# Kernel optimization log

Hardware: AMD Instinct MI355X
Metric: run time of the kernel (lower is better)

The kernel has to match this reference:

```python
import jax, jax.numpy as jnp
import numpy as np

B, C, L = 16, 256, 1024
DIM_U, Q_EMB = 64, 64
INTER = DIM_U * Q_EMB  # 4096
EPS = 1e-5

def setup_inputs() -> dict:
    key = jax.random.key(0)
    ks = jax.random.split(key, 7)
    x = jax.random.normal(ks[0], (B, C, L), dtype=jnp.float32)
    u_i = jax.random.normal(ks[1], (B, DIM_U), dtype=jnp.float32)
    e_qid = jax.random.normal(ks[2], (B, Q_EMB, L), dtype=jnp.float32)
    t = jax.random.normal(ks[3], (B, 1, L), dtype=jnp.float32)
    # nn.Linear weights: (out_features, in_features), Kaiming-uniform-ish init
    wb = 1.0 / np.sqrt(INTER)
    W = jax.random.uniform(ks[4], (2 * C, INTER), jnp.float32, -wb, wb)
    V = jax.random.uniform(ks[5], (2 * C, 1), jnp.float32, -1.0, 1.0)
    bias = jnp.zeros((2 * C,), dtype=jnp.float32)
    return {"x": x, "u_i": u_i, "e_qid": e_qid, "t": t, "W": W, "V": V, "bias": bias}

def reference(x, u_i, e_qid, t, W, V, bias):
    # InstanceNorm1d (affine=False): per-(b,c) stats over L, biased variance
    mean = jnp.mean(x, axis=-1, keepdims=True)
    var = jnp.mean(jnp.square(x - mean), axis=-1, keepdims=True)
    nx = (x - mean) * jax.lax.rsqrt(var + EPS)
    # Bilinear conditioning: interaction[b, u*Q+q, l] = u_i[b,u] * e_qid[b,q,l];
    # style = W @ interaction, fused as a single contraction (no BxINTERxL tensor)
    Wr = W.reshape(2 * C, DIM_U, Q_EMB)
    style = jnp.einsum('bu,bql,cuq->bcl', u_i, e_qid, Wr)  # (B, 2C, L)
    time = jnp.einsum('bol,co->bcl', t, V)                  # (B, 2C, L)
    params = style + time + bias[None, :, None]
    gamma, beta = jnp.split(params, 2, axis=1)
    return (1.0 + gamma) * nx + beta
```

## Files before the change

kernel.cpp:

```cpp
#include <hip/hip_runtime.h>

#define NB 16
#define NC 256
#define NL 1024
#define NQ 64
#define NU 64
#define N2C 512
#define NINTER 4096
#define CT 32
#define LT 128

__global__ __launch_bounds__(256) void calc_A_kernel(
    const float* __restrict__ u_i, const float* __restrict__ W,
    float* __restrict__ A) {
  __shared__ float su[NB * NU];
  __shared__ float part[4][NB][NQ];
  const int t = threadIdx.x;
  const int c2 = blockIdx.x;
  const int q = t & 63;
  const int u4 = t >> 6;

#pragma unroll
  for (int k = 0; k < 4; ++k) su[t + k * 256] = u_i[t + k * 256];
  __syncthreads();

  float acc[NB];
#pragma unroll
  for (int b = 0; b < NB; ++b) acc[b] = 0.0f;

  const float* Wrow = W + c2 * NINTER + u4 * 16 * NQ;
#pragma unroll
  for (int uu = 0; uu < 16; ++uu) {
    const float w = Wrow[uu * NQ + q];
    const int u = u4 * 16 + uu;
#pragma unroll
    for (int b = 0; b < NB; ++b) acc[b] = fmaf(su[b * NU + u], w, acc[b]);
  }
#pragma unroll
  for (int b = 0; b < NB; ++b) part[u4][b][q] = acc[b];
  __syncthreads();

#pragma unroll
  for (int i = 0; i < 4; ++i) {
    const int b = (t >> 6) * 4 + i;
    const float s = part[0][b][q] + part[1][b][q] + part[2][b][q] + part[3][b][q];
    A[(b * N2C + c2) * NQ + q] = s;
  }
}

__global__ __launch_bounds__(256) void stats_kernel(
    const float* __restrict__ x, float* __restrict__ mean,
    float* __restrict__ rstd) {
  const int row = blockIdx.x;
  const int t = threadIdx.x;
  const float4 v = reinterpret_cast<const float4*>(x)[row * (NL / 4) + t];
  float s = v.x + v.y + v.z + v.w;
  float ss = v.x * v.x + v.y * v.y + v.z * v.z + v.w * v.w;
#pragma unroll
  for (int off = 32; off >= 1; off >>= 1) {
    s += __shfl_xor(s, off, 64);
    ss += __shfl_xor(ss, off, 64);
  }
  __shared__ float ls[4], lss[4];
  const int w = t >> 6;
  if ((t & 63) == 0) { ls[w] = s; lss[w] = ss; }
  __syncthreads();
  if (t == 0) {
    const float S = ls[0] + ls[1] + ls[2] + ls[3];
    const float SS = lss[0] + lss[1] + lss[2] + lss[3];
    const float m = S * (1.0f / NL);
    const float var = SS * (1.0f / NL) - m * m;
    mean[row] = m;
    rstd[row] = rsqrtf(var + 1e-5f);
  }
}

__device__ __forceinline__ void fma4(float4& acc, float a, const float4& e) {
  acc.x = fmaf(a, e.x, acc.x);
  acc.y = fmaf(a, e.y, acc.y);
  acc.z = fmaf(a, e.z, acc.z);
  acc.w = fmaf(a, e.w, acc.w);
}

__global__ __launch_bounds__(256) void fused_kernel(
    const float* __restrict__ x, const float* __restrict__ e,
    const float* __restrict__ tt, const float* __restrict__ V,
    const float* __restrict__ bias, const float* __restrict__ A,
    const float* __restrict__ mean, const float* __restrict__ rstd,
    float* __restrict__ out) {
  __shared__ float Ag[CT][NQ];
  __shared__ float Ab[CT][NQ];
  __shared__ float sm[CT], sr[CT];

  const int blk = blockIdx.x;
  const int b = blk >> 6;
  const int ct = (blk >> 3) & 7;
  const int lt = blk & 7;
  const int t = threadIdx.x;
  const int col = t & 31;
  const int rg = t >> 5;

  {
    const float4* Asg =
        reinterpret_cast<const float4*>(A + (b * N2C + ct * CT) * NQ);
    const float4* Asb =
        reinterpret_cast<const float4*>(A + (b * N2C + NC + ct * CT) * NQ);
    float4* Agv = reinterpret_cast<float4*>(&Ag[0][0]);
    float4* Abv = reinterpret_cast<float4*>(&Ab[0][0]);
#pragma unroll
    for (int k = 0; k < 2; ++k) {
      Agv[t + k * 256] = Asg[t + k * 256];
      Abv[t + k * 256] = Asb[t + k * 256];
    }
  }
  if (t < CT) {
    sm[t] = mean[b * NC + ct * CT + t];
    sr[t] = rstd[b * NC + ct * CT + t];
  }
  __syncthreads();

  float4 g[4], p[4];
#pragma unroll
  for (int i = 0; i < 4; ++i) {
    g[i] = make_float4(0.f, 0.f, 0.f, 0.f);
    p[i] = make_float4(0.f, 0.f, 0.f, 0.f);
  }

  const float* ebase = e + b * NQ * NL + lt * LT;
#pragma unroll 4
  for (int q0 = 0; q0 < NQ; q0 += 4) {
    const float4 e0 = reinterpret_cast<const float4*>(ebase + (q0 + 0) * NL)[col];
    const float4 e1 = reinterpret_cast<const float4*>(ebase + (q0 + 1) * NL)[col];
    const float4 e2 = reinterpret_cast<const float4*>(ebase + (q0 + 2) * NL)[col];
    const float4 e3 = reinterpret_cast<const float4*>(ebase + (q0 + 3) * NL)[col];
#pragma unroll
    for (int i = 0; i < 4; ++i) {
      const int r = rg * 4 + i;
      const float4 a = *reinterpret_cast<const float4*>(&Ag[r][q0]);
      fma4(g[i], a.x, e0);
      fma4(g[i], a.y, e1);
      fma4(g[i], a.z, e2);
      fma4(g[i], a.w, e3);
      const float4 c = *reinterpret_cast<const float4*>(&Ab[r][q0]);
      fma4(p[i], c.x, e0);
      fma4(p[i], c.y, e1);
      fma4(p[i], c.z, e2);
      fma4(p[i], c.w, e3);
    }
  }

  const float4 tv = reinterpret_cast<const float4*>(tt + b * NL + lt * LT)[col];
#pragma unroll
  for (int i = 0; i < 4; ++i) {
    const int r = rg * 4 + i;
    const int c = ct * CT + r;
    const float vg = V[c], vb = V[c + NC];
    const float bg = bias[c], bb = bias[c + NC];
    const float m = sm[r], rs = sr[r];
    const float4 xv =
        reinterpret_cast<const float4*>(x + (b * NC + c) * NL + lt * LT)[col];
    float4 o;
    const float gx = 1.0f + g[i].x + fmaf(tv.x, vg, bg);
    const float gy = 1.0f + g[i].y + fmaf(tv.y, vg, bg);
    const float gz = 1.0f + g[i].z + fmaf(tv.z, vg, bg);
    const float gw = 1.0f + g[i].w + fmaf(tv.w, vg, bg);
    o.x = fmaf(gx, (xv.x - m) * rs, p[i].x + fmaf(tv.x, vb, bb));
    o.y = fmaf(gy, (xv.y - m) * rs, p[i].y + fmaf(tv.y, vb, bb));
    o.z = fmaf(gz, (xv.z - m) * rs, p[i].z + fmaf(tv.z, vb, bb));
    o.w = fmaf(gw, (xv.w - m) * rs, p[i].w + fmaf(tv.w, vb, bb));
    reinterpret_cast<float4*>(out + (b * NC + c) * NL + lt * LT)[col] = o;
  }
}

extern "C" void kernel_launch(void* const* d_in, const int* in_sizes, int n_in,
                              void* d_out, int out_size, void* d_ws,
                              size_t ws_size, hipStream_t stream) {
  const float* x = (const float*)d_in[0];
  const float* u_i = (const float*)d_in[1];
  const float* e = (const float*)d_in[2];
  const float* tt = (const float*)d_in[3];
  const float* W = (const float*)d_in[4];
  const float* V = (const float*)d_in[5];
  const float* bias = (const float*)d_in[6];
  float* out = (float*)d_out;

  float* A = (float*)d_ws;
  float* mean = A + NB * N2C * NQ;
  float* rstd = mean + NB * NC;

  calc_A_kernel<<<N2C, 256, 0, stream>>>(u_i, W, A);
  stats_kernel<<<NB * NC, 256, 0, stream>>>(x, mean, rstd);
  fused_kernel<<<NB * 64, 256, 0, stream>>>(x, e, tt, V, bias, A, mean, rstd,
                                            out);
}
```

Before: 108.5 us.

## Fuse instance-norm stats into main kernel and tile full L rows per block

Removes the separate stats kernel. Each fused block now loads 8 full channel rows of x into shared memory, computes mean and rstd there, and reuses the staged x in the epilogue. Blocks now cover the whole L dimension with 8 channels instead of 32 channels by 128 positions. This cuts one launch and the second global read of x. In exchange it uses 32KB of LDS per block, holds 16 float4 accumulators per thread, and launches half as many blocks (512).

```diff
diff --git a/kernel.cpp b/kernel.cpp
--- a/kernel.cpp
+++ b/kernel.cpp
@@ -7,8 +7,7 @@
 #define NU 64
 #define N2C 512
 #define NINTER 4096
-#define CT 32
-#define LT 128
+#define CB 8
 
 __global__ __launch_bounds__(256) void calc_A_kernel(
     const float* __restrict__ u_i, const float* __restrict__ W,
@@ -43,35 +42,9 @@
 #pragma unroll
   for (int i = 0; i < 4; ++i) {
     const int b = (t >> 6) * 4 + i;
-    const float s = part[0][b][q] + part[1][b][q] + part[2][b][q] + part[3][b][q];
+    const float s =
+        part[0][b][q] + part[1][b][q] + part[2][b][q] + part[3][b][q];
     A[(b * N2C + c2) * NQ + q] = s;
-  }
-}
-
-__global__ __launch_bounds__(256) void stats_kernel(
-    const float* __restrict__ x, float* __restrict__ mean,
-    float* __restrict__ rstd) {
-  const int row = blockIdx.x;
-  const int t = threadIdx.x;
-  const float4 v = reinterpret_cast<const float4*>(x)[row * (NL / 4) + t];
-  float s = v.x + v.y + v.z + v.w;
-  float ss = v.x * v.x + v.y * v.y + v.z * v.z + v.w * v.w;
-#pragma unroll
-  for (int off = 32; off >= 1; off >>= 1) {
-    s += __shfl_xor(s, off, 64);
-    ss += __shfl_xor(ss, off, 64);
-  }
-  __shared__ float ls[4], lss[4];
-  const int w = t >> 6;
-  if ((t & 63) == 0) { ls[w] = s; lss[w] = ss; }
-  __syncthreads();
-  if (t == 0) {
-    const float S = ls[0] + ls[1] + ls[2] + ls[3];
-    const float SS = lss[0] + lss[1] + lss[2] + lss[3];
-    const float m = S * (1.0f / NL);
-    const float var = SS * (1.0f / NL) - m * m;
-    mean[row] = m;
-    rstd[row] = rsqrtf(var + 1e-5f);
   }
 }
 
@@ -86,89 +59,90 @@
     const float* __restrict__ x, const float* __restrict__ e,
     const float* __restrict__ tt, const float* __restrict__ V,
     const float* __restrict__ bias, const float* __restrict__ A,
-    const float* __restrict__ mean, const float* __restrict__ rstd,
     float* __restrict__ out) {
-  __shared__ float Ag[CT][NQ];
-  __shared__ float Ab[CT][NQ];
-  __shared__ float sm[CT], sr[CT];
+  __shared__ float xs[CB][NL];
+  __shared__ float As[2 * CB][NQ];
+  __shared__ float sm[CB], sr[CB];
 
   const int blk = blockIdx.x;
-  const int b = blk >> 6;
-  const int ct = (blk >> 3) & 7;
-  const int lt = blk & 7;
+  const int b = blk >> 5;
+  const int c0 = (blk & 31) * CB;
   const int t = threadIdx.x;
-  const int col = t & 31;
-  const int rg = t >> 5;
 
   {
-    const float4* Asg =
-        reinterpret_cast<const float4*>(A + (b * N2C + ct * CT) * NQ);
-    const float4* Asb =
-        reinterpret_cast<const float4*>(A + (b * N2C + NC + ct * CT) * NQ);
-    float4* Agv = reinterpret_cast<float4*>(&Ag[0][0]);
-    float4* Abv = reinterpret_cast<float4*>(&Ab[0][0]);
+    const int fr = t >> 4;
+    const int fc = t & 15;
+    const int ar = (fr < CB) ? (c0 + fr) : (NC + c0 + fr - CB);
+    *reinterpret_cast<float4*>(&As[fr][fc * 4]) =
+        reinterpret_cast<const float4*>(A + (b * N2C + ar) * NQ)[fc];
+  }
+
+  {
+    const int rw = t >> 5;
+    const int cl = t & 31;
+    const float* xrow = x + (b * NC + c0 + rw) * NL;
+    float s = 0.0f, ss = 0.0f;
 #pragma unroll
-    for (int k = 0; k < 2; ++k) {
-      Agv[t + k * 256] = Asg[t + k * 256];
-      Abv[t + k * 256] = Asb[t + k * 256];
+    for (int k = 0; k < 8; ++k) {
+      const float4 v = reinterpret_cast<const float4*>(xrow)[cl + 32 * k];
+      *reinterpret_cast<float4*>(&xs[rw][(cl + 32 * k) * 4]) = v;
+      s += (v.x + v.y) + (v.z + v.w);
+      ss = fmaf(v.x, v.x, fmaf(v.y, v.y, fmaf(v.z, v.z, fmaf(v.w, v.w, ss))));
     }
-  }
-  if (t < CT) {
-    sm[t] = mean[b * NC + ct * CT + t];
-    sr[t] = rstd[b * NC + ct * CT + t];
+#pragma unroll
+    for (int off = 16; off >= 1; off >>= 1) {
+      s += __shfl_xor(s, off, 64);
+      ss += __shfl_xor(ss, off, 64);
+    }
+    if (cl == 0) {
+      const float m = s * (1.0f / NL);
+      sm[rw] = m;
+      sr[rw] = rsqrtf(ss * (1.0f / NL) - m * m + 1e-5f);
+    }
   }
   __syncthreads();
 
-  float4 g[4], p[4];
+  float4 acc[2 * CB];
 #pragma unroll
-  for (int i = 0; i < 4; ++i) {
-    g[i] = make_float4(0.f, 0.f, 0.f, 0.f);
-    p[i] = make_float4(0.f, 0.f, 0.f, 0.f);
-  }
+  for (int r = 0; r < 2 * CB; ++r) acc[r] = make_float4(0.f, 0.f, 0.f, 0.f);
 
-  const float* ebase = e + b * NQ * NL + lt * LT;
-#pragma unroll 4
+  const float* eb = e + b * NQ * NL;
+#pragma unroll 1
   for (int q0 = 0; q0 < NQ; q0 += 4) {
-    const float4 e0 = reinterpret_cast<const float4*>(ebase + (q0 + 0) * NL)[col];
-    const float4 e1 = reinterpret_cast<const float4*>(ebase + (q0 + 1) * NL)[col];
-    const float4 e2 = reinterpret_cast<const float4*>(ebase + (q0 + 2) * NL)[col];
-    const float4 e3 = reinterpret_cast<const float4*>(ebase + (q0 + 3) * NL)[col];
+    const float4 e0 = reinterpret_cast<const float4*>(eb + (q0 + 0) * NL)[t];
+    const float4 e1 = reinterpret_cast<const float4*>(eb + (q0 + 1) * NL)[t];
+    const float4 e2 = reinterpret_cast<const float4*>(eb + (q0 + 2) * NL)[t];
+    const float4 e3 = reinterpret_cast<const float4*>(eb + (q0 + 3) * NL)[t];
 #pragma unroll
-    for (int i = 0; i < 4; ++i) {
-      const int r = rg * 4 + i;
-      const float4 a = *reinterpret_cast<const float4*>(&Ag[r][q0]);
-      fma4(g[i], a.x, e0);
-      fma4(g[i], a.y, e1);
-      fma4(g[i], a.z, e2);
-      fma4(g[i], a.w, e3);
-      const float4 c = *reinterpret_cast<const float4*>(&Ab[r][q0]);
-      fma4(p[i], c.x, e0);
-      fma4(p[i], c.y, e1);
-      fma4(p[i], c.z, e2);
-      fma4(p[i], c.w, e3);
+    for (int r = 0; r < 2 * CB; ++r) {
+      const float4 a = *reinterpret_cast<const float4*>(&As[r][q0]);
+      fma4(acc[r], a.x, e0);
+      fma4(acc[r], a.y, e1);
+      fma4(acc[r], a.z, e2);
+      fma4(acc[r], a.w, e3);
     }
   }
 
-  const float4 tv = reinterpret_cast<const float4*>(tt + b * NL + lt * LT)[col];
+  const float4 tv = reinterpret_cast<const float4*>(tt + b * NL)[t];
 #pragma unroll
-  for (int i = 0; i < 4; ++i) {
-    const int r = rg * 4 + i;
-    const int c = ct * CT + r;
+  for (int r = 0; r < CB; ++r) {
+    const int c = c0 + r;
     const float vg = V[c], vb = V[c + NC];
     const float bg = bias[c], bb = bias[c + NC];
     const float m = sm[r], rs = sr[r];
-    const float4 xv =
-        reinterpret_cast<const float4*>(x + (b * NC + c) * NL + lt * LT)[col];
+    const float4 xv = *reinterpret_cast<const float4*>(&xs[r][t * 4]);
+    const float4 g = acc[r];
+    const float4 p = acc[r + CB];
     float4 o;
-    const float gx = 1.0f + g[i].x + fmaf(tv.x, vg, bg);
-    const float gy = 1.0f + g[i].y + fmaf(tv.y, vg, bg);
-    const float gz = 1.0f + g[i].z + fmaf(tv.z, vg, bg);
-    const float gw = 1.0f + g[i].w + fmaf(tv.w, vg, bg);
-    o.x = fmaf(gx, (xv.x - m) * rs, p[i].x + fmaf(tv.x, vb, bb));
-    o.y = fmaf(gy, (xv.y - m) * rs, p[i].y + fmaf(tv.y, vb, bb));
-    o.z = fmaf(gz, (xv.z - m) * rs, p[i].z + fmaf(tv.z, vb, bb));
-    o.w = fmaf(gw, (xv.w - m) * rs, p[i].w + fmaf(tv.w, vb, bb));
-    reinterpret_cast<float4*>(out + (b * NC + c) * NL + lt * LT)[col] = o;
+    o.x = fmaf(1.0f + g.x + fmaf(tv.x, vg, bg), (xv.x - m) * rs,
+               p.x + fmaf(tv.x, vb, bb));
+    o.y = fmaf(1.0f + g.y + fmaf(tv.y, vg, bg), (xv.y - m) * rs,
+               p.y + fmaf(tv.y, vb, bb));
+    o.z = fmaf(1.0f + g.z + fmaf(tv.z, vg, bg), (xv.z - m) * rs,
+               p.z + fmaf(tv.z, vb, bb));
+    o.w = fmaf(1.0f + g.w + fmaf(tv.w, vg, bg), (xv.w - m) * rs,
+               p.w + fmaf(tv.w, vb, bb));
+    reinterpret_cast<float4*>(out + (b * NC + c) * NL)[t] = o;
   }
 }
 
@@ -185,11 +159,7 @@
   float* out = (float*)d_out;
 
   float* A = (float*)d_ws;
-  float* mean = A + NB * N2C * NQ;
-  float* rstd = mean + NB * NC;
 
   calc_A_kernel<<<N2C, 256, 0, stream>>>(u_i, W, A);
-  stats_kernel<<<NB * NC, 256, 0, stream>>>(x, mean, rstd);
-  fused_kernel<<<NB * 64, 256, 0, stream>>>(x, e, tt, V, bias, A, mean, rstd,
-                                            out);
+  fused_kernel<<<NB * 32, 256, 0, stream>>>(x, e, tt, V, bias, A, out);
 }
```

Result: faster. 103.2 us (-4.9%).
